# Kernel tuning notes

Measured on AMD Instinct MI355X. Metric: run time of the kernel, lower is better.

The kernel has to match this reference:

```python
import jax, jax.numpy as jnp
import numpy as np

B, N, GEO, CLS = 32, 1024, 4, 28
F0 = GEO + CLS          # 32
F1 = F0 * 2             # 64
F2 = F0 * 4             # 128
EPS = 1e-5


def _lin(x, W, b):
    return x @ W.T + b


def _bn(x, g, b):
    # torch BatchNorm1d(element_num) on [B, N, F]: channel dim is N,
    # normalize over (batch, feature) with biased variance (training mode).
    m = x.mean(axis=(0, 2), keepdims=True)
    v = ((x - m) ** 2).mean(axis=(0, 2), keepdims=True)
    return g[None, :, None] * (x - m) * jax.lax.rsqrt(v + EPS) + b[None, :, None]


def _relation(x, Wu, bu, psi, phi, wr):
    # Vectorized form of the triple python loop:
    #   S[b,i,j] = psi*phi * <x_i, x_j>, diagonal excluded
    #   out_i   = wr * (sum_j S[b,i,j] * relu(unary(x_j))) / N + x_i
    n = x.shape[1]
    U = jax.nn.relu(_lin(x, Wu, bu))                       # [B,N,F2]
    S = (psi[0] * phi[0]) * jnp.einsum('bnd,bmd->bnm', x, x)
    S = S * (1.0 - jnp.eye(n, dtype=x.dtype))              # mask i==j
    return wr[0] * (S @ U) / n + x


def setup_inputs() -> dict:
    key = jax.random.key(0)
    ks = iter(jax.random.split(key, 64))

    def W(o, i):
        return jax.random.normal(next(ks), (o, i), jnp.float32) * 0.02

    def bvec(o):
        return jnp.zeros((o,), jnp.float32)

    inp = {'input': jax.random.uniform(next(ks), (B, N, F0), jnp.float32)}
    inp.update(e1_W=W(F1, F0), e1_b=bvec(F1),
               bn1_g=jnp.ones((N,), jnp.float32), bn1_b=bvec(N),
               e2_W=W(F2, F1), e2_b=bvec(F2),
               bn2_g=jnp.ones((N,), jnp.float32), bn2_b=bvec(N),
               e3_W=W(F2, F2), e3_b=bvec(F2))
    for r in (1, 2, 3, 4):
        inp[f'r{r}_W'] = W(F2, F2)
        inp[f'r{r}_b'] = bvec(F2)
        inp[f'r{r}_psi'] = jax.random.uniform(next(ks), (1,), jnp.float32)
        inp[f'r{r}_phi'] = jax.random.uniform(next(ks), (1,), jnp.float32)
        inp[f'r{r}_wr'] = jax.random.uniform(next(ks), (1,), jnp.float32)
    inp.update(d1_W=W(F1, F2), d1_b=bvec(F1),
               dbn_g=jnp.ones((N,), jnp.float32), dbn_b=bvec(N),
               d2_W=W(F0, F1), d2_b=bvec(F0),
               bc_W=W(CLS, F0), bc_b=bvec(CLS),
               bg_W=W(GEO, F0), bg_b=bvec(GEO))
    return inp


def reference(input, e1_W, e1_b, bn1_g, bn1_b, e2_W, e2_b, bn2_g, bn2_b,
              e3_W, e3_b,
              r1_W, r1_b, r1_psi, r1_phi, r1_wr,
              r2_W, r2_b, r2_psi, r2_phi, r2_wr,
              r3_W, r3_b, r3_psi, r3_phi, r3_wr,
              r4_W, r4_b, r4_psi, r4_phi, r4_wr,
              d1_W, d1_b, dbn_g, dbn_b, d2_W, d2_b,
              bc_W, bc_b, bg_W, bg_b):
    out = jax.nn.relu(_bn(_lin(input, e1_W, e1_b), bn1_g, bn1_b))
    out = jax.nn.relu(_bn(_lin(out, e2_W, e2_b), bn2_g, bn2_b))
    enc = jax.nn.sigmoid(_lin(out, e3_W, e3_b))
    x = _relation(enc, r1_W, r1_b, r1_psi, r1_phi, r1_wr)
    x = _relation(x, r2_W, r2_b, r2_psi, r2_phi, r2_wr)
    x = _relation(x, r3_W, r3_b, r3_psi, r3_phi, r3_wr)
    x = _relation(x, r4_W, r4_b, r4_psi, r4_phi, r4_wr)
    out = jax.nn.relu(_bn(_lin(x, d1_W, d1_b), dbn_g, dbn_b))
    out = jax.nn.relu(_lin(out, d2_W, d2_b))
    syn_cls = _lin(out, bc_W, bc_b)
    syn_geo = _lin(out, bg_W, bg_b)
    return jnp.concatenate((syn_cls, syn_geo), axis=2)
```

## Files before the change

kernel.cpp:

```cpp
#include <hip/hip_runtime.h>
#include <hip/hip_bf16.h>


typedef __hip_bfloat16 bf16;
typedef unsigned short ushort_t;
typedef float v4f __attribute__((ext_vector_type(4)));
typedef short v8s __attribute__((ext_vector_type(8)));
#define MFMA_BF16 __builtin_amdgcn_mfma_f32_16x16x32_bf16

#define NB 32
#define NN 1024

__device__ __forceinline__ float ldin(const void* p, size_t i, int f32){
    return f32 ? ((const float*)p)[i] : __bfloat162float(((const bf16*)p)[i]);
}
__device__ __forceinline__ float bf2f(ushort_t u){
    return __uint_as_float((unsigned)u << 16);
}
__device__ __forceinline__ ushort_t f2bf(float v){
    bf16 h = __float2bfloat16(v);
    ushort_t s; __builtin_memcpy(&s, &h, 2);
    return s;
}
__device__ __forceinline__ void unpack8(uint4 v, float* f){
    f[0] = __uint_as_float(v.x << 16);
    f[1] = __uint_as_float(v.x & 0xffff0000u);
    f[2] = __uint_as_float(v.y << 16);
    f[3] = __uint_as_float(v.y & 0xffff0000u);
    f[4] = __uint_as_float(v.z << 16);
    f[5] = __uint_as_float(v.z & 0xffff0000u);
    f[6] = __uint_as_float(v.w << 16);
    f[7] = __uint_as_float(v.w & 0xffff0000u);
}

__device__ __forceinline__ int detect_dev(const void* inp){
    __shared__ int sflag;
    int t = threadIdx.x;
    if (t < 64){
        unsigned v = ((const unsigned*)inp)[t];
        unsigned long long m = __ballot((v & 0x80008000u) != 0u);
        if (t == 0) sflag = (__popcll(m) > 4) ? 1 : 0;
    }
    __syncthreads();
    return sflag;
}

struct PrepArgs {
    const void* w[11];
    int K[11], O[11], off[11];
};

__global__ __launch_bounds__(256) void k_prep(PrepArgs a, float* __restrict__ wpf,
                                              ushort_t* __restrict__ whi, ushort_t* __restrict__ wlo,
                                              const void* __restrict__ detin){
    int f32 = detect_dev(detin);
    int s = blockIdx.y;
    int idx = blockIdx.x*256 + threadIdx.x;
    if (s < 6){
        int K = a.K[s], O = a.O[s];
        if (idx >= K*O) return;
        int k = idx / O, j = idx - k*O;
        wpf[a.off[s] + idx] = ldin(a.w[s], (size_t)j*K + k, f32);
    } else {
        if (idx >= 16384) return;
        int n = idx >> 7, k = idx & 127;
        float v = ldin(a.w[s], (size_t)n*128 + k, f32);
        ushort_t h = f2bf(v);
        ushort_t l = f2bf(v - bf2f(h));
        int di = (s - 6)*16384 + ((k >> 3)*128 + n)*8 + (k & 7);
        whi[di] = h; wlo[di] = l;
    }
}

template<int K, int O, bool EXTIN>
__global__ __launch_bounds__(128) void k_bnlin(
    const void* __restrict__ xin, const float* __restrict__ Wt,
    const void* __restrict__ bias, const void* __restrict__ bng,
    const void* __restrict__ bnb, ushort_t* __restrict__ out,
    const void* __restrict__ detin)
{
    int f32 = detect_dev(detin);
    constexpr int BR  = O/16;
    constexpr int NBT = 32/BR;
    constexpr int G   = K/8;
    __shared__ __align__(16) float wt[K*O];
    __shared__ __align__(16) float xst[2][K*36];
    int t = threadIdx.x;
    int w = t >> 6, lane = t & 63;
    int n = blockIdx.x*2 + w;

    for (int i = t; i < K*O/4; i += 128)
        ((float4*)wt)[i] = ((const float4*)Wt)[i];
    for (int i = lane; i < 32*G; i += 64){
        int b = i / G, g = i - b*G;
        float f[8];
        if (EXTIN && f32){
            const float* src = (const float*)xin + ((size_t)b*NN + n)*K + g*8;
            float4 v0 = ((const float4*)src)[0];
            float4 v1 = ((const float4*)src)[1];
            f[0]=v0.x; f[1]=v0.y; f[2]=v0.z; f[3]=v0.w;
            f[4]=v1.x; f[5]=v1.y; f[6]=v1.z; f[7]=v1.w;
        } else {
            uint4 v = *(const uint4*)((const ushort_t*)xin + ((size_t)b*NN + n)*K + (size_t)g*8);
            unpack8(v, f);
        }
        #pragma unroll
        for (int j=0;j<8;j++) xst[w][(g*8+j)*36 + b] = f[j];
    }
    __syncthreads();

    int bt = lane % NBT, jt = lane / NBT;
    int b0 = bt*BR, j0 = jt*8;
    const float* xw = xst[w];
    float acc[BR][8];
    #pragma unroll
    for (int i=0;i<BR;i++)
        #pragma unroll
        for (int j=0;j<8;j++) acc[i][j] = 0.f;

    for (int k = 0; k < K; k++){
        float xv[BR], wv[8];
        #pragma unroll
        for (int i=0;i<BR;i+=4)
            *(float4*)&xv[i] = *(const float4*)&xw[k*36 + b0 + i];
        *(float4*)&wv[0] = *(const float4*)&wt[k*O + j0];
        *(float4*)&wv[4] = *(const float4*)&wt[k*O + j0 + 4];
        #pragma unroll
        for (int i=0;i<BR;i++)
            #pragma unroll
            for (int j=0;j<8;j++) acc[i][j] = fmaf(xv[i], wv[j], acc[i][j]);
    }

    float bj[8];
    #pragma unroll
    for (int j=0;j<8;j++) bj[j] = ldin(bias, j0+j, f32);
    float s1 = 0.f, s2 = 0.f;
    #pragma unroll
    for (int i=0;i<BR;i++)
        #pragma unroll
        for (int j=0;j<8;j++){
            float a = acc[i][j] + bj[j];
            acc[i][j] = a; s1 += a; s2 = fmaf(a, a, s2);
        }
    #pragma unroll
    for (int off = 32; off > 0; off >>= 1){
        s1 += __shfl_down(s1, off);
        s2 += __shfl_down(s2, off);
    }
    s1 = __shfl(s1, 0); s2 = __shfl(s2, 0);
    const float M = 32.f * O;
    float m  = s1 / M;
    float vv = s2 / M - m*m;
    float rs = rsqrtf(vv + 1e-5f);
    float gv = ldin(bng, n, f32), bv = ldin(bnb, n, f32);
    #pragma unroll
    for (int i=0;i<BR;i++){
        union { uint4 u; ushort_t s[8]; } pk;
        #pragma unroll
        for (int j=0;j<8;j++)
            pk.s[j] = f2bf(fmaxf(fmaf(gv*(acc[i][j]-m), rs, bv), 0.f));
        *(uint4*)(out + ((size_t)(b0+i)*NN + n)*O + j0) = pk.u;
    }
}


__device__ __forceinline__ void tail_stage_x(ushort_t* xs, ushort_t* xt,
                                             const float o[2][16],
                                             int w, int col, int quad){
    #pragma unroll
    for (int nt=0;nt<2;nt++){
        int n = w*32 + nt*16 + col;
        #pragma unroll
        for (int m=0;m<4;m++){
            union { uint2 u2; ushort_t s[4]; } pk;
            #pragma unroll
            for (int reg=0;reg<4;reg++){
                int r = m*16 + quad*4 + reg;
                ushort_t hv = f2bf(o[nt][m*4+reg]);
                xs[((n>>3)*64 + r)*8 + (n&7)] = hv;
                pk.s[reg] = hv;
            }
            *(uint2*)&xt[n*64 + m*16 + quad*4] = pk.u2;
        }
    }
}

__device__ __forceinline__ void tail_write_A(const ushort_t* xs, ushort_t* A,
                                             size_t row0, int t){
    uint4* dst = (uint4*)(A + row0*128);
    #pragma unroll
    for (int c = 0; c < 4; c++){
        int i = t + c*256;
        int r = i >> 4, kg = i & 15;
        dst[i] = *(const uint4*)&xs[(kg*64 + r)*8];
    }
}

__device__ __forceinline__ void tail_lin_relu_T(ushort_t* xs, ushort_t* xt,
    ushort_t* UT, const ushort_t* Whi, const ushort_t* Wlo, const void* bias,
    float* dvec, ushort_t* Tp,
    size_t row0, int b, int rbase, int t, int w, int col, int quad, int f32)
{
    if (t < 64){
        float s = 0.f;
        #pragma unroll 8
        for (int k=0;k<128;k++){
            float v = bf2f(xs[((k>>3)*64 + t)*8 + (k&7)]);
            s = fmaf(v, v, s);
        }
        dvec[row0 + t] = s;
    }
    v4f acc[4][2];
    #pragma unroll
    for (int m=0;m<4;m++)
        #pragma unroll
        for (int nt=0;nt<2;nt++) acc[m][nt] = (v4f){0.f,0.f,0.f,0.f};
    #pragma unroll
    for (int kt = 0; kt < 4; kt++){
        int kg = kt*4 + quad;
        v8s a[4], bh[2], bl[2];
        #pragma unroll
        for (int nt=0;nt<2;nt++){
            int n = w*32 + nt*16 + col;
            bh[nt] = *(const v8s*)&Whi[(kg*128 + n)*8];
            bl[nt] = *(const v8s*)&Wlo[(kg*128 + n)*8];
        }
        #pragma unroll
        for (int m=0;m<4;m++)
            a[m] = *(const v8s*)&xs[(kg*64 + m*16 + col)*8];
        #pragma unroll
        for (int m=0;m<4;m++)
            #pragma unroll
            for (int nt=0;nt<2;nt++){
                acc[m][nt] = MFMA_BF16(a[m], bh[nt], acc[m][nt], 0, 0, 0);
                acc[m][nt] = MFMA_BF16(a[m], bl[nt], acc[m][nt], 0, 0, 0);
            }
    }
    float u[2][16];
    #pragma unroll
    for (int nt=0;nt<2;nt++){
        int n = w*32 + nt*16 + col;
        float bn = ldin(bias, n, f32);
        #pragma unroll
        for (int m=0;m<4;m++)
            #pragma unroll
            for (int reg=0;reg<4;reg++)
                u[nt][m*4+reg] = fmaxf(acc[m][nt][reg] + bn, 0.f);
    }
    __syncthreads();
    #pragma unroll
    for (int nt=0;nt<2;nt++){
        int n = w*32 + nt*16 + col;
        #pragma unroll
        for (int m=0;m<4;m++){
            union { uint2 u2; ushort_t s[4]; } pk;
            #pragma unroll
            for (int reg=0;reg<4;reg++)
                pk.s[reg] = f2bf(u[nt][m*4+reg]);
            *(uint2*)&xs[n*64 + m*16 + quad*4] = pk.u2;
        }
    }
    __syncthreads();
    #pragma unroll
    for (int c = 0; c < 4; c++){
        int i = t + c*256;
        int n = i >> 3, sg = i & 7;
        *(uint4*)&UT[((size_t)b*128 + n)*1024 + rbase + sg*8] =
            *(const uint4*)&xs[n*64 + sg*8];
    }
    v4f tacc[4][4];
    #pragma unroll
    for (int m=0;m<4;m++)
        #pragma unroll
        for (int q=0;q<4;q++) tacc[m][q] = (v4f){0.f,0.f,0.f,0.f};
    int wn = (w & 1)*64, wc = (w >> 1)*64;
    #pragma unroll
    for (int kt = 0; kt < 2; kt++){
        int kg = kt*4 + quad;
        v8s a[4], bb[4];
        #pragma unroll
        for (int m=0;m<4;m++)
            a[m] = *(const v8s*)&xs[(wn + m*16 + col)*64 + kg*8];
        #pragma unroll
        for (int q=0;q<4;q++)
            bb[q] = *(const v8s*)&xt[(wc + q*16 + col)*64 + kg*8];
        #pragma unroll
        for (int m=0;m<4;m++)
            #pragma unroll
            for (int q=0;q<4;q++)
                tacc[m][q] = MFMA_BF16(a[m], bb[q], tacc[m][q], 0, 0, 0);
    }
    int s16 = (int)((row0 >> 6) & 15);
    ushort_t* dst = Tp + ((size_t)(s16*NB + b) << 14);
    #pragma unroll
    for (int m=0;m<4;m++)
        #pragma unroll
        for (int q=0;q<4;q++){
            int c = wc + q*16 + col;
            union { uint2 u2; ushort_t s[4]; } pk;
            #pragma unroll
            for (int reg=0;reg<4;reg++)
                pk.s[reg] = f2bf(tacc[m][q][reg]);
            *(uint2*)&dst[c*128 + wn + m*16 + quad*4] = pk.u2;
        }
}

__global__ __launch_bounds__(256) void k_linfuse0(
    const ushort_t* __restrict__ xin,
    const ushort_t* __restrict__ W3h, const ushort_t* __restrict__ W3l,
    const void* __restrict__ b3,
    const ushort_t* __restrict__ W1h, const ushort_t* __restrict__ W1l,
    const void* __restrict__ b1,
    ushort_t* __restrict__ A, ushort_t* __restrict__ UT,
    float* __restrict__ dvec, ushort_t* __restrict__ Tp,
    const void* __restrict__ detin)
{
    __shared__ __align__(16) ushort_t xs[8192];
    __shared__ __align__(16) ushort_t xt[8192];
    int f32 = detect_dev(detin);
    int t = threadIdx.x;
    size_t row0 = (size_t)blockIdx.x * 64;
    int b = (int)(row0 >> 10), rbase = (int)(row0 & 1023);
    {
        const uint4* src = (const uint4*)(xin + row0*128);
        #pragma unroll
        for (int c = 0; c < 4; c++){
            int i = t + c*256;
            int r = i >> 4, kg = i & 15;
            *(uint4*)&xs[(kg*64 + r)*8] = src[i];
        }
    }
    __syncthreads();
    int w = t >> 6, lane = t & 63;
    int col = lane & 15, quad = lane >> 4;
    v4f acc[4][2];
    #pragma unroll
    for (int m=0;m<4;m++)
        #pragma unroll
        for (int nt=0;nt<2;nt++) acc[m][nt] = (v4f){0.f,0.f,0.f,0.f};
    #pragma unroll
    for (int kt = 0; kt < 4; kt++){
        int kg = kt*4 + quad;
        v8s a[4], bh[2], bl[2];
        #pragma unroll
        for (int nt=0;nt<2;nt++){
            int n = w*32 + nt*16 + col;
            bh[nt] = *(const v8s*)&W3h[(kg*128 + n)*8];
            bl[nt] = *(const v8s*)&W3l[(kg*128 + n)*8];
        }
        #pragma unroll
        for (int m=0;m<4;m++)
            a[m] = *(const v8s*)&xs[(kg*64 + m*16 + col)*8];
        #pragma unroll
        for (int m=0;m<4;m++)
            #pragma unroll
            for (int nt=0;nt<2;nt++){
                acc[m][nt] = MFMA_BF16(a[m], bh[nt], acc[m][nt], 0, 0, 0);
                acc[m][nt] = MFMA_BF16(a[m], bl[nt], acc[m][nt], 0, 0, 0);
            }
    }
    float o[2][16];
    #pragma unroll
    for (int nt=0;nt<2;nt++){
        int n = w*32 + nt*16 + col;
        float bn = ldin(b3, n, f32);
        #pragma unroll
        for (int m=0;m<4;m++)
            #pragma unroll
            for (int reg=0;reg<4;reg++){
                float v = acc[m][nt][reg] + bn;
                o[nt][m*4+reg] = 1.f/(1.f+expf(-v));
            }
    }
    __syncthreads();
    tail_stage_x(xs, xt, o, w, col, quad);
    __syncthreads();
    tail_write_A(xs, A, row0, t);
    tail_lin_relu_T(xs, xt, UT, W1h, W1l, b1, dvec, Tp,
                    row0, b, rbase, t, w, col, quad, f32);
}

__global__ __launch_bounds__(256) void k_tredb(const ushort_t* __restrict__ Tp,
                                               ushort_t* __restrict__ Thi, ushort_t* __restrict__ Tlo){
    int tau = blockIdx.x*256 + threadIdx.x;
    int b = tau >> 11;
    int j2 = tau & 2047;
    int cg = j2 >> 7, n = j2 & 127;
    float sum[8] = {0,0,0,0,0,0,0,0};
    #pragma unroll
    for (int s = 0; s < 16; s++){
        const ushort_t* src = Tp + ((size_t)(s*NB + b) << 14) + cg*8*128 + n;
        #pragma unroll
        for (int cc = 0; cc < 8; cc++)
            sum[cc] += bf2f(src[cc*128]);
    }
    union { uint4 u; ushort_t s[8]; } ph, pl;
    #pragma unroll
    for (int cc = 0; cc < 8; cc++){
        ushort_t h = f2bf(sum[cc]);
        ph.s[cc] = h;
        pl.s[cc] = f2bf(sum[cc] - bf2f(h));
    }
    size_t di = ((size_t)b << 14) + ((size_t)cg*128 + n)*8;
    *(uint4*)&Thi[di] = ph.u;
    *(uint4*)&Tlo[di] = pl.u;
}

template<int LAST>
__global__ __launch_bounds__(256) void k_relfuse(
    ushort_t* __restrict__ x, ushort_t* __restrict__ UT,
    const ushort_t* __restrict__ Thi, const ushort_t* __restrict__ Tlo,
    float* __restrict__ dvec,
    const void* __restrict__ psi, const void* __restrict__ phi, const void* __restrict__ wr,
    const ushort_t* __restrict__ Wnh, const ushort_t* __restrict__ Wnl,
    const void* __restrict__ bnext, ushort_t* __restrict__ Tp,
    const void* __restrict__ detin)
{
    __shared__ __align__(16) ushort_t xs[8192];
    __shared__ __align__(16) ushort_t xt[8192];
    int f32 = detect_dev(detin);
    int t = threadIdx.x;
    size_t row0 = (size_t)blockIdx.x * 64;
    int b = (int)(row0 >> 10), rbase = (int)(row0 & 1023);
    {
        const uint4* src = (const uint4*)(x + row0*128);
        #pragma unroll
        for (int c = 0; c < 4; c++){
            int i = t + c*256;
            int r = i >> 4, kg = i & 15;
            *(uint4*)&xs[(kg*64 + r)*8] = src[i];
        }
    }
    __syncthreads();
    float alpha = ldin(wr,0,f32) * ldin(psi,0,f32) * ldin(phi,0,f32) * (1.f/1024.f);
    int w = t >> 6, lane = t & 63;
    int col = lane & 15, quad = lane >> 4;
    const ushort_t* sh = Thi + ((size_t)b << 14);
    const ushort_t* sl = Tlo + ((size_t)b << 14);
    v4f acc[4][2];
    #pragma unroll
    for (int m=0;m<4;m++)
        #pragma unroll
        for (int nt=0;nt<2;nt++) acc[m][nt] = (v4f){0.f,0.f,0.f,0.f};
    #pragma unroll
    for (int kt = 0; kt < 4; kt++){
        int kg = kt*4 + quad;
        v8s a[4], bh[2], bl[2];
        #pragma unroll
        for (int nt=0;nt<2;nt++){
            int n = w*32 + nt*16 + col;
            bh[nt] = *(const v8s*)&sh[(kg*128 + n)*8];
            bl[nt] = *(const v8s*)&sl[(kg*128 + n)*8];
        }
        #pragma unroll
        for (int m=0;m<4;m++)
            a[m] = *(const v8s*)&xs[(kg*64 + m*16 + col)*8];
        #pragma unroll
        for (int m=0;m<4;m++)
            #pragma unroll
            for (int nt=0;nt<2;nt++){
                acc[m][nt] = MFMA_BF16(a[m], bh[nt], acc[m][nt], 0, 0, 0);
                acc[m][nt] = MFMA_BF16(a[m], bl[nt], acc[m][nt], 0, 0, 0);
            }
    }
    float o[2][16];
    #pragma unroll
    for (int m=0;m<4;m++){
        float4 d4 = *(const float4*)&dvec[row0 + m*16 + quad*4];
        const float* dr = (const float*)&d4;
        #pragma unroll
        for (int nt=0;nt<2;nt++){
            int n = w*32 + nt*16 + col;
            uint2 uu = *(const uint2*)&UT[((size_t)b*128 + n)*1024 + rbase + m*16 + quad*4];
            float uf[4];
            uf[0] = __uint_as_float(uu.x << 16);
            uf[1] = __uint_as_float(uu.x & 0xffff0000u);
            uf[2] = __uint_as_float(uu.y << 16);
            uf[3] = __uint_as_float(uu.y & 0xffff0000u);
            #pragma unroll
            for (int reg=0;reg<4;reg++){
                int r = m*16 + quad*4 + reg;
                float xv = bf2f(xs[((n>>3)*64 + r)*8 + (n&7)]);
                o[nt][m*4+reg] = fmaf(alpha, acc[m][nt][reg] - dr[reg]*uf[reg], xv);
            }
        }
    }
    __syncthreads();
    tail_stage_x(xs, xt, o, w, col, quad);
    __syncthreads();
    tail_write_A(xs, x, row0, t);
    if (!LAST)
        tail_lin_relu_T(xs, xt, UT, Wnh, Wnl, bnext, dvec, Tp,
                        row0, b, rbase, t, w, col, quad, f32);
}

__global__ __launch_bounds__(256) void k_dec2(
    const ushort_t* __restrict__ x,
    const float* __restrict__ W2t, const void* __restrict__ b2,
    const float* __restrict__ Wct, const void* __restrict__ bcb,
    const float* __restrict__ Wgt, const void* __restrict__ bgb,
    void* __restrict__ out, const void* __restrict__ detin)
{
    int f32 = detect_dev(detin);
    __shared__ __align__(16) float w2[64*32];
    __shared__ __align__(16) float wc[32*28];
    __shared__ __align__(16) float wg[32*4];
    __shared__ __align__(16) float xsd[8][64];
    __shared__ float hs[8][33];
    int t = threadIdx.x;
    for (int i=t;i<512;i+=256)  ((float4*)w2)[i] = ((const float4*)W2t)[i];
    if (t < 224) ((float4*)wc)[t] = ((const float4*)Wct)[t];
    if (t < 32)  ((float4*)wg)[t] = ((const float4*)Wgt)[t];
    int j = t & 31, r = t >> 5;
    for (int tile = blockIdx.x; tile < 4096; tile += 512){
        size_t row0 = (size_t)tile * 8;
        __syncthreads();
        if (t < 64){
            int row = t >> 3, seg = t & 7;
            uint4 v = *(const uint4*)&x[(row0 + row)*64 + seg*8];
            float f[8]; unpack8(v, f);
            *(float4*)&xsd[row][seg*8]   = make_float4(f[0],f[1],f[2],f[3]);
            *(float4*)&xsd[row][seg*8+4] = make_float4(f[4],f[5],f[6],f[7]);
        }
        __syncthreads();
        float a = ldin(b2, j, f32);
        #pragma unroll 8
        for (int k=0;k<64;k++) a = fmaf(xsd[r][k], w2[k*32 + j], a);
        hs[r][j] = fmaxf(a, 0.f);
        __syncthreads();
        float o;
        if (j < 28){
            o = ldin(bcb, j, f32);
            #pragma unroll
            for (int k=0;k<32;k++) o = fmaf(hs[r][k], wc[k*28 + j], o);
        } else {
            int jj = j - 28;
            o = ldin(bgb, jj, f32);
            #pragma unroll
            for (int k=0;k<32;k++) o = fmaf(hs[r][k], wg[k*4 + jj], o);
        }
        size_t oi = (row0 + r)*32 + j;
        if (f32) ((float*)out)[oi] = o;
        else     ((ushort_t*)out)[oi] = f2bf(o);
    }
}

enum { O_E1=0, O_E2=2048, O_D1=10240, O_D2=18432, O_BC=20480, O_BG=21376 };

extern "C" void kernel_launch(void* const* d_in, const int* in_sizes, int n_in,
                              void* d_out, int out_size, void* d_ws, size_t ws_size,
                              hipStream_t stream)
{
    (void)in_sizes; (void)n_in; (void)out_size; (void)ws_size;
    const void* input = d_in[0];
    const void* e1_W = d_in[1];  const void* e1_b = d_in[2];
    const void* bn1_g = d_in[3]; const void* bn1_b = d_in[4];
    const void* e2_W = d_in[5];  const void* e2_b = d_in[6];
    const void* bn2_g = d_in[7]; const void* bn2_b = d_in[8];
    const void* e3_W = d_in[9];  const void* e3_b = d_in[10];
    const void *rW[4], *rb[4], *rpsi[4], *rphi[4], *rwr[4];
    for (int r = 0; r < 4; r++){
        rW[r]   = d_in[11 + r*5 + 0];
        rb[r]   = d_in[11 + r*5 + 1];
        rpsi[r] = d_in[11 + r*5 + 2];
        rphi[r] = d_in[11 + r*5 + 3];
        rwr[r]  = d_in[11 + r*5 + 4];
    }
    const void* d1_W = d_in[31]; const void* d1_b = d_in[32];
    const void* dbn_g = d_in[33];const void* dbn_b = d_in[34];
    const void* d2_W = d_in[35]; const void* d2_b = d_in[36];
    const void* bc_W = d_in[37]; const void* bc_b = d_in[38];
    const void* bg_W = d_in[39]; const void* bg_b = d_in[40];

    float*    ws_f = (float*)d_ws;
    float*    wpf  = ws_f;
    float*    dd   = ws_f + 21504;
    ushort_t* whi  = (ushort_t*)(ws_f + 54272);
    ushort_t* wlo  = (ushort_t*)(ws_f + 95232);
    ushort_t* Thi  = (ushort_t*)(ws_f + 136192);
    ushort_t* Tlo  = (ushort_t*)(ws_f + 398336);
    ushort_t* Tp   = (ushort_t*)(ws_f + 660480);
    ushort_t* A    = (ushort_t*)(ws_f + 4854784);
    ushort_t* UT   = (ushort_t*)(ws_f + 6951936);
    ushort_t* E2   = (ushort_t*)(ws_f + 9049088);
    ushort_t* Cenc = A;
    ushort_t* Cdec = UT;

    PrepArgs pa;
    const void* srcs[11] = {e1_W, e2_W, d1_W, d2_W, bc_W, bg_W,
                            e3_W, rW[0], rW[1], rW[2], rW[3]};
    const int  Ks[11]   = {32,64,128,64,32,32, 128,128,128,128,128};
    const int  Os[11]   = {64,128,64,32,28,4,  128,128,128,128,128};
    const int  offs[11] = {O_E1,O_E2,O_D1,O_D2,O_BC,O_BG, 0,0,0,0,0};
    for (int i=0;i<11;i++){ pa.w[i]=srcs[i]; pa.K[i]=Ks[i]; pa.O[i]=Os[i]; pa.off[i]=offs[i]; }

    k_prep<<<dim3(64,11), 256, 0, stream>>>(pa, wpf, whi, wlo, input);
    k_bnlin<32,64,true><<<512, 128, 0, stream>>>(input, wpf+O_E1, e1_b, bn1_g, bn1_b, Cenc, input);
    k_bnlin<64,128,false><<<512, 128, 0, stream>>>(Cenc, wpf+O_E2, e2_b, bn2_g, bn2_b, E2, input);
    k_linfuse0<<<512, 256, 0, stream>>>(E2, whi, wlo, e3_b,
                                        whi + 16384, wlo + 16384, rb[0],
                                        A, UT, dd, Tp, input);

    for (int r = 0; r < 4; r++){
        k_tredb<<<256, 256, 0, stream>>>(Tp, Thi, Tlo);
        if (r < 3)
            k_relfuse<0><<<512, 256, 0, stream>>>(A, UT, Thi, Tlo, dd,
                rpsi[r], rphi[r], rwr[r],
                whi + (size_t)(2+r)*16384, wlo + (size_t)(2+r)*16384, rb[r+1], Tp, input);
        else
            k_relfuse<1><<<512, 256, 0, stream>>>(A, UT, Thi, Tlo, dd,
                rpsi[r], rphi[r], rwr[r], whi, wlo, rb[r], Tp, input);
    }

    k_bnlin<128,64,false><<<512, 128, 0, stream>>>(A, wpf+O_D1, d1_b, dbn_g, dbn_b, Cdec, input);
    k_dec2<<<512, 256, 0, stream>>>(Cdec, wpf+O_D2, d2_b, wpf+O_BC, bc_b, wpf+O_BG, bg_b, d_out, input);
}
```

Measured before the change: 320.0 us.

## Fuse encoder BN-linear stages, pad LDS stride, stage UT tile in shared memory

Merges the first two linear+batchnorm+relu encoder stages into one kernel, so the intermediate activation stays in shared memory instead of making a round trip through global memory, and one launch is dropped. The transposed LDS tiles now use a padded row stride of 72 to reduce bank conflicts on the MFMA operand reads. The relation-fuse kernel loads its UT tile into shared memory with a coalesced copy up front, replacing scattered global reads in the epilogue. In exchange, the fused kernel uses more shared memory per block (about 50KB, mostly the two weight tables), which may lower occupancy.

```diff
diff --git a/kernel.cpp b/kernel.cpp
--- a/kernel.cpp
+++ b/kernel.cpp
@@ -10,6 +10,7 @@
 
 #define NB 32
 #define NN 1024
+#define XSTRIDE 72
 
 __device__ __forceinline__ float ldin(const void* p, size_t i, int f32){
     return f32 ? ((const float*)p)[i] : __bfloat162float(((const bf16*)p)[i]);
@@ -72,9 +73,145 @@
     }
 }
 
-template<int K, int O, bool EXTIN>
+__global__ __launch_bounds__(128) void k_bnlin12(
+    const void* __restrict__ xin,
+    const float* __restrict__ Wt1, const void* __restrict__ b1v,
+    const void* __restrict__ g1, const void* __restrict__ bb1,
+    const float* __restrict__ Wt2, const void* __restrict__ b2v,
+    const void* __restrict__ g2, const void* __restrict__ bb2,
+    ushort_t* __restrict__ out, const void* __restrict__ detin)
+{
+    int f32 = detect_dev(detin);
+    __shared__ __align__(16) float wt1[32*64];
+    __shared__ __align__(16) float wt2[64*128];
+    __shared__ __align__(16) float xst[2][32*36];
+    __shared__ __align__(16) float cst[2][64*36];
+    int t = threadIdx.x;
+    int w = t >> 6, lane = t & 63;
+    int n = blockIdx.x*2 + w;
+
+    for (int i = t; i < 32*64/4; i += 128)
+        ((float4*)wt1)[i] = ((const float4*)Wt1)[i];
+    for (int i = t; i < 64*128/4; i += 128)
+        ((float4*)wt2)[i] = ((const float4*)Wt2)[i];
+    for (int i = lane; i < 32*4; i += 64){
+        int b = i >> 2, g = i & 3;
+        float f[8];
+        if (f32){
+            const float* src = (const float*)xin + ((size_t)b*NN + n)*32 + g*8;
+            float4 v0 = ((const float4*)src)[0];
+            float4 v1 = ((const float4*)src)[1];
+            f[0]=v0.x; f[1]=v0.y; f[2]=v0.z; f[3]=v0.w;
+            f[4]=v1.x; f[5]=v1.y; f[6]=v1.z; f[7]=v1.w;
+        } else {
+            uint4 v = *(const uint4*)((const ushort_t*)xin + ((size_t)b*NN + n)*32 + (size_t)g*8);
+            unpack8(v, f);
+        }
+        #pragma unroll
+        for (int j=0;j<8;j++) xst[w][(g*8+j)*36 + b] = f[j];
+    }
+    __syncthreads();
+
+    {
+        int b0 = (lane & 7)*4, j0 = (lane >> 3)*8;
+        float acc[4][8];
+        #pragma unroll
+        for (int i=0;i<4;i++)
+            #pragma unroll
+            for (int j=0;j<8;j++) acc[i][j] = 0.f;
+        for (int k = 0; k < 32; k++){
+            float xv[4], wv[8];
+            *(float4*)&xv[0] = *(const float4*)&xst[w][k*36 + b0];
+            *(float4*)&wv[0] = *(const float4*)&wt1[k*64 + j0];
+            *(float4*)&wv[4] = *(const float4*)&wt1[k*64 + j0 + 4];
+            #pragma unroll
+            for (int i=0;i<4;i++)
+                #pragma unroll
+                for (int j=0;j<8;j++) acc[i][j] = fmaf(xv[i], wv[j], acc[i][j]);
+        }
+        float bj[8];
+        #pragma unroll
+        for (int j=0;j<8;j++) bj[j] = ldin(b1v, j0+j, f32);
+        float s1 = 0.f, s2 = 0.f;
+        #pragma unroll
+        for (int i=0;i<4;i++)
+            #pragma unroll
+            for (int j=0;j<8;j++){
+                float a = acc[i][j] + bj[j];
+                acc[i][j] = a; s1 += a; s2 = fmaf(a, a, s2);
+            }
+        #pragma unroll
+        for (int off = 32; off > 0; off >>= 1){
+            s1 += __shfl_down(s1, off);
+            s2 += __shfl_down(s2, off);
+        }
+        s1 = __shfl(s1, 0); s2 = __shfl(s2, 0);
+        float m  = s1 / 2048.f;
+        float vv = s2 / 2048.f - m*m;
+        float rs = rsqrtf(vv + 1e-5f);
+        float gv = ldin(g1, n, f32), bv = ldin(bb1, n, f32);
+        #pragma unroll
+        for (int i=0;i<4;i++)
+            #pragma unroll
+            for (int j=0;j<8;j++)
+                cst[w][(j0+j)*36 + b0+i] =
+                    fmaxf(fmaf(gv*(acc[i][j]-m), rs, bv), 0.f);
+    }
+    __syncthreads();
+
+    {
+        int b0 = (lane & 3)*8, j0 = (lane >> 2)*8;
+        float acc[8][8];
+        #pragma unroll
+        for (int i=0;i<8;i++)
+            #pragma unroll
+            for (int j=0;j<8;j++) acc[i][j] = 0.f;
+        for (int k = 0; k < 64; k++){
+            float xv[8], wv[8];
+            *(float4*)&xv[0] = *(const float4*)&cst[w][k*36 + b0];
+            *(float4*)&xv[4] = *(const float4*)&cst[w][k*36 + b0 + 4];
+            *(float4*)&wv[0] = *(const float4*)&wt2[k*128 + j0];
+            *(float4*)&wv[4] = *(const float4*)&wt2[k*128 + j0 + 4];
+            #pragma unroll
+            for (int i=0;i<8;i++)
+                #pragma unroll
+                for (int j=0;j<8;j++) acc[i][j] = fmaf(xv[i], wv[j], acc[i][j]);
+        }
+        float bj[8];
+        #pragma unroll
+        for (int j=0;j<8;j++) bj[j] = ldin(b2v, j0+j, f32);
+        float s1 = 0.f, s2 = 0.f;
+        #pragma unroll
+        for (int i=0;i<8;i++)
+            #pragma unroll
+            for (int j=0;j<8;j++){
+                float a = acc[i][j] + bj[j];
+                acc[i][j] = a; s1 += a; s2 = fmaf(a, a, s2);
+            }
+        #pragma unroll
+        for (int off = 32; off > 0; off >>= 1){
+            s1 += __shfl_down(s1, off);
+            s2 += __shfl_down(s2, off);
+        }
+        s1 = __shfl(s1, 0); s2 = __shfl(s2, 0);
+        float m  = s1 / 4096.f;
+        float vv = s2 / 4096.f - m*m;
+        float rs = rsqrtf(vv + 1e-5f);
+        float gv = ldin(g2, n, f32), bv = ldin(bb2, n, f32);
+        #pragma unroll
+        for (int i=0;i<8;i++){
+            union { uint4 u; ushort_t s[8]; } pk;
+            #pragma unroll
+            for (int j=0;j<8;j++)
+                pk.s[j] = f2bf(fmaxf(fmaf(gv*(acc[i][j]-m), rs, bv), 0.f));
+            *(uint4*)(out + ((size_t)(b0+i)*NN + n)*128 + j0) = pk.u;
+        }
+    }
+}
+
+template<int K, int O>
 __global__ __launch_bounds__(128) void k_bnlin(
-    const void* __restrict__ xin, const float* __restrict__ Wt,
+    const ushort_t* __restrict__ xin, const float* __restrict__ Wt,
     const void* __restrict__ bias, const void* __restrict__ bng,
     const void* __restrict__ bnb, ushort_t* __restrict__ out,
     const void* __restrict__ detin)
@@ -94,16 +231,8 @@
     for (int i = lane; i < 32*G; i += 64){
         int b = i / G, g = i - b*G;
         float f[8];
-        if (EXTIN && f32){
-            const float* src = (const float*)xin + ((size_t)b*NN + n)*K + g*8;
-            float4 v0 = ((const float4*)src)[0];
-            float4 v1 = ((const float4*)src)[1];
-            f[0]=v0.x; f[1]=v0.y; f[2]=v0.z; f[3]=v0.w;
-            f[4]=v1.x; f[5]=v1.y; f[6]=v1.z; f[7]=v1.w;
-        } else {
-            uint4 v = *(const uint4*)((const ushort_t*)xin + ((size_t)b*NN + n)*K + (size_t)g*8);
-            unpack8(v, f);
-        }
+        uint4 v = *(const uint4*)(xin + ((size_t)b*NN + n)*K + (size_t)g*8);
+        unpack8(v, f);
         #pragma unroll
         for (int j=0;j<8;j++) xst[w][(g*8+j)*36 + b] = f[j];
     }
@@ -180,7 +309,7 @@
                 xs[((n>>3)*64 + r)*8 + (n&7)] = hv;
                 pk.s[reg] = hv;
             }
-            *(uint2*)&xt[n*64 + m*16 + quad*4] = pk.u2;
+            *(uint2*)&xt[n*XSTRIDE + m*16 + quad*4] = pk.u2;
         }
     }
 }
@@ -257,7 +386,7 @@
             #pragma unroll
             for (int reg=0;reg<4;reg++)
                 pk.s[reg] = f2bf(u[nt][m*4+reg]);
-            *(uint2*)&xs[n*64 + m*16 + quad*4] = pk.u2;
+            *(uint2*)&xs[n*XSTRIDE + m*16 + quad*4] = pk.u2;
         }
     }
     __syncthreads();
@@ -266,7 +395,7 @@
         int i = t + c*256;
         int n = i >> 3, sg = i & 7;
         *(uint4*)&UT[((size_t)b*128 + n)*1024 + rbase + sg*8] =
-            *(const uint4*)&xs[n*64 + sg*8];
+            *(const uint4*)&xs[n*XSTRIDE + sg*8];
     }
     v4f tacc[4][4];
     #pragma unroll
@@ -280,10 +409,10 @@
         v8s a[4], bb[4];
         #pragma unroll
         for (int m=0;m<4;m++)
-            a[m] = *(const v8s*)&xs[(wn + m*16 + col)*64 + kg*8];
+            a[m] = *(const v8s*)&xs[(wn + m*16 + col)*XSTRIDE + kg*8];
         #pragma unroll
         for (int q=0;q<4;q++)
-            bb[q] = *(const v8s*)&xt[(wc + q*16 + col)*64 + kg*8];
+            bb[q] = *(const v8s*)&xt[(wc + q*16 + col)*XSTRIDE + kg*8];
         #pragma unroll
         for (int m=0;m<4;m++)
             #pragma unroll
@@ -315,8 +444,8 @@
     float* __restrict__ dvec, ushort_t* __restrict__ Tp,
     const void* __restrict__ detin)
 {
-    __shared__ __align__(16) ushort_t xs[8192];
-    __shared__ __align__(16) ushort_t xt[8192];
+    __shared__ __align__(16) ushort_t xs[128*XSTRIDE];
+    __shared__ __align__(16) ushort_t xt[128*XSTRIDE];
     int f32 = detect_dev(detin);
     int t = threadIdx.x;
     size_t row0 = (size_t)blockIdx.x * 64;
@@ -416,19 +545,23 @@
     const void* __restrict__ bnext, ushort_t* __restrict__ Tp,
     const void* __restrict__ detin)
 {
-    __shared__ __align__(16) ushort_t xs[8192];
-    __shared__ __align__(16) ushort_t xt[8192];
+    __shared__ __align__(16) ushort_t xs[128*XSTRIDE];
+    __shared__ __align__(16) ushort_t xt[128*XSTRIDE];
     int f32 = detect_dev(detin);
     int t = threadIdx.x;
     size_t row0 = (size_t)blockIdx.x * 64;
     int b = (int)(row0 >> 10), rbase = (int)(row0 & 1023);
     {
         const uint4* src = (const uint4*)(x + row0*128);
+        const ushort_t* utb = UT + (size_t)b*128*1024 + rbase;
         #pragma unroll
         for (int c = 0; c < 4; c++){
             int i = t + c*256;
             int r = i >> 4, kg = i & 15;
             *(uint4*)&xs[(kg*64 + r)*8] = src[i];
+            int n2 = i >> 3, sg = i & 7;
+            *(uint4*)&xt[n2*XSTRIDE + sg*8] =
+                *(const uint4*)&utb[(size_t)n2*1024 + sg*8];
         }
     }
     __syncthreads();
@@ -471,17 +604,12 @@
         #pragma unroll
         for (int nt=0;nt<2;nt++){
             int n = w*32 + nt*16 + col;
-            uint2 uu = *(const uint2*)&UT[((size_t)b*128 + n)*1024 + rbase + m*16 + quad*4];
-            float uf[4];
-            uf[0] = __uint_as_float(uu.x << 16);
-            uf[1] = __uint_as_float(uu.x & 0xffff0000u);
-            uf[2] = __uint_as_float(uu.y << 16);
-            uf[3] = __uint_as_float(uu.y & 0xffff0000u);
             #pragma unroll
             for (int reg=0;reg<4;reg++){
                 int r = m*16 + quad*4 + reg;
+                float ufv = bf2f(xt[n*XSTRIDE + r]);
                 float xv = bf2f(xs[((n>>3)*64 + r)*8 + (n&7)]);
-                o[nt][m*4+reg] = fmaf(alpha, acc[m][nt][reg] - dr[reg]*uf[reg], xv);
+                o[nt][m*4+reg] = fmaf(alpha, acc[m][nt][reg] - dr[reg]*ufv, xv);
             }
         }
     }
@@ -583,7 +711,6 @@
     ushort_t* A    = (ushort_t*)(ws_f + 4854784);
     ushort_t* UT   = (ushort_t*)(ws_f + 6951936);
     ushort_t* E2   = (ushort_t*)(ws_f + 9049088);
-    ushort_t* Cenc = A;
     ushort_t* Cdec = UT;
 
     PrepArgs pa;
@@ -595,8 +722,10 @@
     for (int i=0;i<11;i++){ pa.w[i]=srcs[i]; pa.K[i]=Ks[i]; pa.O[i]=Os[i]; pa.off[i]=offs[i]; }
 
     k_prep<<<dim3(64,11), 256, 0, stream>>>(pa, wpf, whi, wlo, input);
-    k_bnlin<32,64,true><<<512, 128, 0, stream>>>(input, wpf+O_E1, e1_b, bn1_g, bn1_b, Cenc, input);
-    k_bnlin<64,128,false><<<512, 128, 0, stream>>>(Cenc, wpf+O_E2, e2_b, bn2_g, bn2_b, E2, input);
+    k_bnlin12<<<512, 128, 0, stream>>>(input,
+                                       wpf+O_E1, e1_b, bn1_g, bn1_b,
+                                       wpf+O_E2, e2_b, bn2_g, bn2_b,
+                                       E2, input);
     k_linfuse0<<<512, 256, 0, stream>>>(E2, whi, wlo, e3_b,
                                         whi + 16384, wlo + 16384, rb[0],
                                         A, UT, dd, Tp, input);
@@ -612,6 +741,6 @@
                 rpsi[r], rphi[r], rwr[r], whi, wlo, rb[r], Tp, input);
     }
 
-    k_bnlin<128,64,false><<<512, 128, 0, stream>>>(A, wpf+O_D1, d1_b, dbn_g, dbn_b, Cdec, input);
+    k_bnlin<128,64><<<512, 128, 0, stream>>>(A, wpf+O_D1, d1_b, dbn_g, dbn_b, Cdec, input);
     k_dec2<<<512, 256, 0, stream>>>(Cdec, wpf+O_D2, d2_b, wpf+O_BC, bc_b, wpf+O_BG, bg_b, d_out, input);
 }
```

Result: faster. 293.8 us (-8.2%).
